# Performance work log

Measured on AMD Instinct MI355X. Metric: run time of the kernel, lower is better.

The kernel has to match this reference:

```python
import jax, jax.numpy as jnp
import numpy as np

DIM = 256
NUM_HEADS = 8
WH, WW = 7, 7
N = WH * WW
HEAD_DIM = DIM // NUM_HEADS
SCALE = HEAD_DIM ** -0.5
B_ = 4096
NW = 64  # windows per image


def _relative_position_index():
    # Swin relative position index: (N, N) int32 in [0, (2Wh-1)*(2Ww-1))
    coords = np.stack(np.meshgrid(np.arange(WH), np.arange(WW), indexing='ij'))  # (2, Wh, Ww)
    cf = coords.reshape(2, -1)  # (2, N)
    rel = cf[:, :, None] - cf[:, None, :]  # (2, N, N)
    rel = rel.transpose(1, 2, 0).copy()
    rel[:, :, 0] += WH - 1
    rel[:, :, 1] += WW - 1
    rel[:, :, 0] *= 2 * WW - 1
    return jnp.asarray(rel.sum(-1), dtype=jnp.int32)  # (N, N)


def setup_inputs() -> dict:
    key = jax.random.key(0)
    ks = jax.random.split(key, 7)
    x = jax.random.normal(ks[0], (B_, N, DIM), dtype=jnp.float32)
    mask = jax.random.normal(ks[1], (NW, N, N), dtype=jnp.float32)
    qkv_w = jax.random.normal(ks[2], (3 * DIM, DIM), dtype=jnp.float32) * 0.02
    qkv_b = jnp.zeros((3 * DIM,), dtype=jnp.float32)
    proj_w = jax.random.normal(ks[3], (DIM, DIM), dtype=jnp.float32) * 0.02
    proj_b = jnp.zeros((DIM,), dtype=jnp.float32)
    bias_table = jax.random.normal(ks[4], ((2 * WH - 1) * (2 * WW - 1), NUM_HEADS), dtype=jnp.float32) * 0.02
    rel_index = _relative_position_index()
    return {"x": x, "mask": mask, "qkv_w": qkv_w, "qkv_b": qkv_b,
            "proj_w": proj_w, "proj_b": proj_b, "bias_table": bias_table,
            "rel_index": rel_index}


def reference(x, mask, qkv_w, qkv_b, proj_w, proj_b, bias_table, rel_index):
    Bw, n, c = x.shape
    # qkv projection: (B_, N, 3C) -> (3, B_, nH, N, hd)
    qkv = (x @ qkv_w.T + qkv_b).reshape(Bw, n, 3, NUM_HEADS, HEAD_DIM)
    qkv = qkv.transpose(2, 0, 3, 1, 4)
    q, k, v = qkv[0], qkv[1], qkv[2]
    attn = jnp.einsum('bhqd,bhkd->bhqk', q * SCALE, k)  # (B_, nH, N, N)
    # gathered relative position bias: (nH, N, N)
    rpb = bias_table[rel_index.reshape(-1)].reshape(n, n, NUM_HEADS).transpose(2, 0, 1)
    attn = attn + rpb[None]
    # window mask: reshape batch into (B, nW) and broadcast mask per-window
    nW = mask.shape[0]
    attn = attn.reshape(Bw // nW, nW, NUM_HEADS, n, n) + mask[None, :, None]
    attn = attn.reshape(Bw, NUM_HEADS, n, n)
    attn = jax.nn.softmax(attn, axis=-1)
    out = jnp.einsum('bhqk,bhkd->bhqd', attn, v)  # (B_, nH, N, hd)
    out = out.transpose(0, 2, 1, 3).reshape(Bw, n, c)
    return out @ proj_w.T + proj_b
```

## Files before the change

### kernel.cpp

```cpp
#include <hip/hip_runtime.h>
#include <hip/hip_bf16.h>

typedef __bf16 bf16;
typedef __bf16 bf16x2 __attribute__((ext_vector_type(2)));
typedef __bf16 bf16x8 __attribute__((ext_vector_type(8)));
typedef float  f32x4  __attribute__((ext_vector_type(4)));
typedef float  f32x8  __attribute__((ext_vector_type(8)));

#define MFMA16(A,B,C) __builtin_amdgcn_mfma_f32_16x16x32_bf16((A),(B),(C),0,0,0)

constexpr int   N_TOK = 49;
constexpr int   DIM_C = 256;
constexpr float SCALE = 0.17677669529663687f;

constexpr int VT         = 25088;
constexpr int PAD_BASE   = VT + 256 * 56;
constexpr int SMEM_ELEMS = PAD_BASE + 512;

constexpr size_t CB_BYTES    = 64ull * 8 * 64 * 64 * 4;
constexpr int    QKVW_ELEMS  = 768 * 256;
constexpr int    PROJW_ELEMS = 256 * 256;

__global__ __launch_bounds__(256) void build_cb_kernel(
    const float* __restrict__ bias_table, const float* __restrict__ mask,
    const int* __restrict__ rel_index, float* __restrict__ cb) {
  int idx = blockIdx.x * 256 + threadIdx.x;
  int j = idx & 63, m = (idx >> 6) & 63, h = (idx >> 12) & 7, w = idx >> 15;
  float v = 0.f;
  if (j < N_TOK && m < N_TOK)
    v = bias_table[rel_index[m * 49 + j] * 8 + h] + mask[(w * 49 + m) * 49 + j];
  cb[idx] = v;
}

__global__ __launch_bounds__(256) void cvt_w_kernel(
    const float* __restrict__ qkv_w, const float* __restrict__ proj_w,
    bf16* __restrict__ qkv_wb, bf16* __restrict__ proj_wb) {
  int i = blockIdx.x * 256 + threadIdx.x;
  if (i < QKVW_ELEMS) qkv_wb[i] = (bf16)qkv_w[i];
  else                proj_wb[i - QKVW_ELEMS] = (bf16)proj_w[i - QKVW_ELEMS];
}

__global__ __launch_bounds__(512, 4) void win_attn_kernel(
    const float* __restrict__ x, const bf16* __restrict__ qkv_wb,
    const float* __restrict__ qkv_b, const bf16* __restrict__ proj_wb,
    const float* __restrict__ proj_b, const float* __restrict__ cb,
    float* __restrict__ out) {
  __shared__ bf16 smem[SMEM_ELEMS];

  const int beta  = blockIdx.x;
  const int w_idx = beta >> 6;
  const int img   = beta & 63;
  const int b     = img * 64 + w_idx;
  const int tid   = threadIdx.x;
  const int wv    = tid >> 6;
  const int l     = tid & 63;
  const int l15   = l & 15, lgp = l >> 4;

  const f32x4 fzero = {0.f, 0.f, 0.f, 0.f};

  if (tid < 512) smem[PAD_BASE + tid] = (bf16)0.f;
  if (tid < 224) {
    int d = 224 + tid / 7, j = 49 + tid % 7;
    smem[VT + d * 56 + j] = (bf16)0.f;
  }

  const float* xg = x + (size_t)b * (N_TOK * DIM_C);
  for (int c = tid; c < (N_TOK * DIM_C / 8); c += 512) {
    int m = c >> 5, k0 = (c & 31) * 8;
    f32x8 f = *reinterpret_cast<const f32x8*>(xg + m * 256 + k0);
    bf16x8 v;
#pragma unroll
    for (int e = 0; e < 8; ++e) v[e] = (bf16)f[e];
    *reinterpret_cast<bf16x8*>(&smem[VT + m * 256 + (k0 ^ ((m & 7) << 3))]) = v;
  }
  __syncthreads();

  {
    f32x4 acc[4][4];
#pragma unroll
    for (int i = 0; i < 4; ++i)
      for (int mt = 0; mt < 4; ++mt) acc[i][mt] = fzero;
    for (int k0 = 0; k0 < 8; ++k0) {
      const int kk = k0 * 32 + lgp * 8;
      bf16x8 XBf[4];
#pragma unroll
      for (int mt = 0; mt < 4; ++mt) {
        int m = mt * 16 + l15; int mc = m < N_TOK ? m : 48;
        XBf[mt] = *reinterpret_cast<const bf16x8*>(
            &smem[VT + mc * 256 + (kk ^ ((mc & 7) << 3))]);
      }
#pragma unroll
      for (int i = 0; i < 4; ++i) {
        int c = (4 * wv + i) * 16 + l15;
        bf16x8 Aw = *reinterpret_cast<const bf16x8*>(qkv_wb + c * DIM_C + kk);
#pragma unroll
        for (int mt = 0; mt < 4; ++mt) acc[i][mt] = MFMA16(Aw, XBf[mt], acc[i][mt]);
      }
    }
#pragma unroll
    for (int i = 0; i < 4; ++i) {
      int ct = 4 * wv + i;
      int c0 = ct * 16 + lgp * 4;
      f32x4 qb = *reinterpret_cast<const f32x4*>(qkv_b + c0);
      float sc = (ct < 16) ? SCALE : 1.0f;
#pragma unroll
      for (int mt = 0; mt < 4; ++mt) {
        int m = mt * 16 + l15;
        if (m < N_TOK) {
          float v0 = (acc[i][mt][0] + qb[0]) * sc;
          float v1 = (acc[i][mt][1] + qb[1]) * sc;
          float v2 = (acc[i][mt][2] + qb[2]) * sc;
          float v3 = (acc[i][mt][3] + qb[3]) * sc;
          int base = m * 512 + (c0 ^ ((m & 7) << 3));
          *reinterpret_cast<bf16x2*>(&smem[base])     = bf16x2{(bf16)v0, (bf16)v1};
          *reinterpret_cast<bf16x2*>(&smem[base + 2]) = bf16x2{(bf16)v2, (bf16)v3};
        }
      }
    }
  }

  {
    f32x4 accv[2][4];
#pragma unroll
    for (int i = 0; i < 2; ++i)
      for (int mt = 0; mt < 4; ++mt) accv[i][mt] = fzero;
    for (int k0 = 0; k0 < 8; ++k0) {
      const int kk = k0 * 32 + lgp * 8;
      bf16x8 XA[4];
#pragma unroll
      for (int mt = 0; mt < 4; ++mt) {
        int m = mt * 16 + l15; int mc = m < N_TOK ? m : 48;
        XA[mt] = *reinterpret_cast<const bf16x8*>(
            &smem[VT + mc * 256 + (kk ^ ((mc & 7) << 3))]);
      }
#pragma unroll
      for (int i = 0; i < 2; ++i) {
        int c = (32 + 2 * wv + i) * 16 + l15;
        bf16x8 Bw = *reinterpret_cast<const bf16x8*>(qkv_wb + c * DIM_C + kk);
#pragma unroll
        for (int mt = 0; mt < 4; ++mt) accv[i][mt] = MFMA16(XA[mt], Bw, accv[i][mt]);
      }
    }
    __syncthreads();
#pragma unroll
    for (int i = 0; i < 2; ++i) {
      int dd = (2 * wv + i) * 16 + l15;
      float qb = qkv_b[512 + dd];
#pragma unroll
      for (int mt = 0; mt < 4; ++mt) {
#pragma unroll
        for (int r = 0; r < 4; ++r) {
          int m = mt * 16 + lgp * 4 + r;
          if (m < N_TOK) smem[VT + dd * 56 + m] = (bf16)(accv[i][mt][r] + qb);
        }
      }
    }
  }
  __syncthreads();

  const int h = wv;
  {
    bf16x8 Vf[2][2];
#pragma unroll
    for (int dt = 0; dt < 2; ++dt)
#pragma unroll
      for (int ks = 0; ks < 2; ++ks) {
        int d = h * 32 + dt * 16 + l15;
        Vf[dt][ks] = *reinterpret_cast<const bf16x8*>(
            &smem[VT + d * 56 + ks * 32 + lgp * 8]);
      }
    bf16x8 Ak[4];
#pragma unroll
    for (int jt = 0; jt < 4; ++jt) {
      int j = jt * 16 + l15; int jr = j < N_TOK ? j : 48;
      Ak[jt] = *reinterpret_cast<const bf16x8*>(
          &smem[jr * 512 + ((256 + h * 32 + lgp * 8) ^ ((jr & 7) << 3))]);
    }
    const float* cbp = cb + ((size_t)(w_idx * 8 + h)) * 4096;

#pragma unroll
    for (int mt = 0; mt < 4; ++mt) {
      int mrow = mt * 16 + l15;
      int mc = mrow < N_TOK ? mrow : 48;
      bf16x8 Bq = *reinterpret_cast<const bf16x8*>(
          &smem[mc * 512 + ((h * 32 + lgp * 8) ^ ((mc & 7) << 3))]);
      f32x4 s4[4];
#pragma unroll
      for (int jt = 0; jt < 4; ++jt) s4[jt] = MFMA16(Ak[jt], Bq, fzero);

      float e[4][4];
#pragma unroll
      for (int jt = 0; jt < 4; ++jt) {
        f32x4 cb4 = *reinterpret_cast<const f32x4*>(
            cbp + mrow * 64 + jt * 16 + lgp * 4);
#pragma unroll
        for (int r = 0; r < 4; ++r) {
          float v = s4[jt][r] + cb4[r];
          if (jt == 3) {
            if (r == 0) v = (lgp == 0) ? v : -3.0e38f;
            else        v = -3.0e38f;
          }
          e[jt][r] = v;
        }
      }
      float mx = e[0][0];
#pragma unroll
      for (int jt = 0; jt < 4; ++jt)
#pragma unroll
        for (int r = 0; r < 4; ++r) mx = fmaxf(mx, e[jt][r]);
      mx = fmaxf(mx, __shfl_xor(mx, 16));
      mx = fmaxf(mx, __shfl_xor(mx, 32));
      float sum = 0.f;
#pragma unroll
      for (int jt = 0; jt < 4; ++jt)
#pragma unroll
        for (int r = 0; r < 4; ++r) {
          float ex = __expf(e[jt][r] - mx);
          e[jt][r] = ex;
          sum += ex;
        }
      sum += __shfl_xor(sum, 16);
      sum += __shfl_xor(sum, 32);
      float rinv = 1.0f / sum;

      if (mrow < N_TOK) {
#pragma unroll
        for (int jt = 0; jt < 4; ++jt) {
          int jc0 = jt * 16 + lgp * 4;
          int cc  = (jt < 2) ? (h * 32 + jc0) : (224 + h * 32 + jc0);
          int base = mrow * 512 + (cc ^ ((mrow & 7) << 3));
          *reinterpret_cast<bf16x2*>(&smem[base]) =
              bf16x2{(bf16)e[jt][0], (bf16)e[jt][1]};
          *reinterpret_cast<bf16x2*>(&smem[base + 2]) =
              bf16x2{(bf16)e[jt][2], (bf16)e[jt][3]};
        }
      }
      f32x4 pv[2] = {fzero, fzero};
#pragma unroll
      for (int ks = 0; ks < 2; ++ks) {
        int j0 = ks * 32 + lgp * 8;
        int cc = ((ks == 0) ? (h * 32) : (224 + h * 32)) + j0;
        bf16x8 Bp = *reinterpret_cast<const bf16x8*>(
            &smem[mc * 512 + (cc ^ ((mc & 7) << 3))]);
#pragma unroll
        for (int dt = 0; dt < 2; ++dt) pv[dt] = MFMA16(Vf[dt][ks], Bp, pv[dt]);
      }
      if (mrow < N_TOK) {
#pragma unroll
        for (int dt = 0; dt < 2; ++dt) {
          float a0 = pv[dt][0] * rinv, a1 = pv[dt][1] * rinv;
          float a2 = pv[dt][2] * rinv, a3 = pv[dt][3] * rinv;
          int cc0 = 256 + h * 32 + dt * 16 + lgp * 4;
          int base = mrow * 512 + (cc0 ^ ((mrow & 7) << 3));
          *reinterpret_cast<bf16x2*>(&smem[base])     = bf16x2{(bf16)a0, (bf16)a1};
          *reinterpret_cast<bf16x2*>(&smem[base + 2]) = bf16x2{(bf16)a2, (bf16)a3};
        }
      }
    }
  }
  __syncthreads();

  f32x4 acc2[2][4];
#pragma unroll
  for (int ci = 0; ci < 2; ++ci)
    for (int mt = 0; mt < 4; ++mt) acc2[ci][mt] = fzero;
  for (int k0 = 0; k0 < 8; ++k0) {
    const int kk = k0 * 32 + lgp * 8;
    bf16x8 Bao[4];
#pragma unroll
    for (int mt = 0; mt < 4; ++mt) {
      int m = mt * 16 + l15; int mc = m < N_TOK ? m : 48;
      Bao[mt] = *reinterpret_cast<const bf16x8*>(
          &smem[mc * 512 + ((256 + kk) ^ ((mc & 7) << 3))]);
    }
#pragma unroll
    for (int ci = 0; ci < 2; ++ci) {
      int c = (2 * wv + ci) * 16 + l15;
      bf16x8 Aw = *reinterpret_cast<const bf16x8*>(proj_wb + c * DIM_C + kk);
#pragma unroll
      for (int mt = 0; mt < 4; ++mt) acc2[ci][mt] = MFMA16(Aw, Bao[mt], acc2[ci][mt]);
    }
  }
  float* ob = out + (size_t)b * (N_TOK * DIM_C);
#pragma unroll
  for (int ci = 0; ci < 2; ++ci) {
    int c0 = (2 * wv + ci) * 16 + lgp * 4;
    f32x4 pb = *reinterpret_cast<const f32x4*>(proj_b + c0);
#pragma unroll
    for (int mt = 0; mt < 4; ++mt) {
      int mrow = mt * 16 + l15;
      if (mrow < N_TOK) {
        f32x4 o;
#pragma unroll
        for (int r = 0; r < 4; ++r) o[r] = acc2[ci][mt][r] + pb[r];
        *reinterpret_cast<f32x4*>(ob + mrow * 256 + c0) = o;
      }
    }
  }
}

extern "C" void kernel_launch(void* const* d_in, const int* in_sizes, int n_in,
                              void* d_out, int out_size, void* d_ws, size_t ws_size,
                              hipStream_t stream) {
  const float* x          = (const float*)d_in[0];
  const float* mask       = (const float*)d_in[1];
  const float* qkv_w      = (const float*)d_in[2];
  const float* qkv_b      = (const float*)d_in[3];
  const float* proj_w     = (const float*)d_in[4];
  const float* proj_b     = (const float*)d_in[5];
  const float* bias_table = (const float*)d_in[6];
  const int*   rel_index  = (const int*)d_in[7];

  float* cb      = (float*)d_ws;
  bf16*  qkv_wb  = (bf16*)((char*)d_ws + CB_BYTES);
  bf16*  proj_wb = (bf16*)((char*)d_ws + CB_BYTES + QKVW_ELEMS * 2);

  hipLaunchKernelGGL(build_cb_kernel, dim3(8192), dim3(256), 0, stream,
                     bias_table, mask, rel_index, cb);
  hipLaunchKernelGGL(cvt_w_kernel, dim3(1024), dim3(256), 0, stream,
                     qkv_w, proj_w, qkv_wb, proj_wb);
  hipLaunchKernelGGL(win_attn_kernel, dim3(4096), dim3(512), 0, stream,
                     x, qkv_wb, qkv_b, proj_wb, proj_b, cb, (float*)d_out);
}
```

Measured before the change: 427.9 us.

## Keep per-head Q/K/V and P in registers via cross-lane shuffles instead of LDS

```diff
diff --git a/kernel.cpp b/kernel.cpp
--- a/kernel.cpp
+++ b/kernel.cpp
@@ -2,7 +2,7 @@
 #include <hip/hip_bf16.h>
 
 typedef __bf16 bf16;
-typedef __bf16 bf16x2 __attribute__((ext_vector_type(2)));
+typedef __bf16 bf16x4v __attribute__((ext_vector_type(4)));
 typedef __bf16 bf16x8 __attribute__((ext_vector_type(8)));
 typedef float  f32x4  __attribute__((ext_vector_type(4)));
 typedef float  f32x8  __attribute__((ext_vector_type(8)));
@@ -13,9 +13,7 @@
 constexpr int   DIM_C = 256;
 constexpr float SCALE = 0.17677669529663687f;
 
-constexpr int VT         = 25088;
-constexpr int PAD_BASE   = VT + 256 * 56;
-constexpr int SMEM_ELEMS = PAD_BASE + 512;
+constexpr int SMEM_ELEMS = N_TOK * 256;
 
 constexpr size_t CB_BYTES    = 64ull * 8 * 64 * 64 * 4;
 constexpr int    QKVW_ELEMS  = 768 * 256;
@@ -40,6 +38,28 @@
   else                proj_wb[i - QKVW_ELEMS] = (bf16)proj_w[i - QKVW_ELEMS];
 }
 
+__device__ __forceinline__ bf16x8 repack8(f32x4 Ta, f32x4 Tb, int l15, int lgp) {
+  const int s0 = l15 + ((lgp & 1) << 5);
+  const bool hi = (lgp & 2) != 0;
+  bf16x8 F;
+#pragma unroll
+  for (int r = 0; r < 4; ++r) {
+    float a0 = __shfl(Ta[r], s0);
+    float b0 = __shfl(Tb[r], s0);
+    F[r] = (bf16)(hi ? b0 : a0);
+    float a1 = __shfl(Ta[r], s0 + 16);
+    float b1 = __shfl(Tb[r], s0 + 16);
+    F[r + 4] = (bf16)(hi ? b1 : a1);
+  }
+  return F;
+}
+
+__device__ __forceinline__ bf16x8 tile_read(const bf16* sm, int mt, int l15, int kk) {
+  int m = mt * 16 + l15;
+  int mc = m < N_TOK ? m : 48;
+  return *reinterpret_cast<const bf16x8*>(&sm[mc * 256 + (kk ^ ((mc & 7) << 3))]);
+}
+
 __global__ __launch_bounds__(512, 4) void win_attn_kernel(
     const float* __restrict__ x, const bf16* __restrict__ qkv_wb,
     const float* __restrict__ qkv_b, const bf16* __restrict__ proj_wb,
@@ -55,14 +75,9 @@
   const int wv    = tid >> 6;
   const int l     = tid & 63;
   const int l15   = l & 15, lgp = l >> 4;
+  const int h     = wv;
 
   const f32x4 fzero = {0.f, 0.f, 0.f, 0.f};
-
-  if (tid < 512) smem[PAD_BASE + tid] = (bf16)0.f;
-  if (tid < 224) {
-    int d = 224 + tid / 7, j = 49 + tid % 7;
-    smem[VT + d * 56 + j] = (bf16)0.f;
-  }
 
   const float* xg = x + (size_t)b * (N_TOK * DIM_C);
   for (int c = tid; c < (N_TOK * DIM_C / 8); c += 512) {
@@ -71,191 +86,145 @@
     bf16x8 v;
 #pragma unroll
     for (int e = 0; e < 8; ++e) v[e] = (bf16)f[e];
-    *reinterpret_cast<bf16x8*>(&smem[VT + m * 256 + (k0 ^ ((m & 7) << 3))]) = v;
+    *reinterpret_cast<bf16x8*>(&smem[m * 256 + (k0 ^ ((m & 7) << 3))]) = v;
   }
   __syncthreads();
 
+  bf16x8 Qf[4], Kf[4];
   {
-    f32x4 acc[4][4];
-#pragma unroll
-    for (int i = 0; i < 4; ++i)
-      for (int mt = 0; mt < 4; ++mt) acc[i][mt] = fzero;
+    f32x4 dq[2][4], dk[2][4];
+#pragma unroll
+    for (int i = 0; i < 2; ++i)
+      for (int mt = 0; mt < 4; ++mt) { dq[i][mt] = fzero; dk[i][mt] = fzero; }
+#pragma unroll 2
     for (int k0 = 0; k0 < 8; ++k0) {
       const int kk = k0 * 32 + lgp * 8;
-      bf16x8 XBf[4];
-#pragma unroll
-      for (int mt = 0; mt < 4; ++mt) {
-        int m = mt * 16 + l15; int mc = m < N_TOK ? m : 48;
-        XBf[mt] = *reinterpret_cast<const bf16x8*>(
-            &smem[VT + mc * 256 + (kk ^ ((mc & 7) << 3))]);
-      }
-#pragma unroll
-      for (int i = 0; i < 4; ++i) {
-        int c = (4 * wv + i) * 16 + l15;
-        bf16x8 Aw = *reinterpret_cast<const bf16x8*>(qkv_wb + c * DIM_C + kk);
-#pragma unroll
-        for (int mt = 0; mt < 4; ++mt) acc[i][mt] = MFMA16(Aw, XBf[mt], acc[i][mt]);
-      }
-    }
-#pragma unroll
-    for (int i = 0; i < 4; ++i) {
-      int ct = 4 * wv + i;
-      int c0 = ct * 16 + lgp * 4;
-      f32x4 qb = *reinterpret_cast<const f32x4*>(qkv_b + c0);
-      float sc = (ct < 16) ? SCALE : 1.0f;
-#pragma unroll
-      for (int mt = 0; mt < 4; ++mt) {
-        int m = mt * 16 + l15;
-        if (m < N_TOK) {
-          float v0 = (acc[i][mt][0] + qb[0]) * sc;
-          float v1 = (acc[i][mt][1] + qb[1]) * sc;
-          float v2 = (acc[i][mt][2] + qb[2]) * sc;
-          float v3 = (acc[i][mt][3] + qb[3]) * sc;
-          int base = m * 512 + (c0 ^ ((m & 7) << 3));
-          *reinterpret_cast<bf16x2*>(&smem[base])     = bf16x2{(bf16)v0, (bf16)v1};
-          *reinterpret_cast<bf16x2*>(&smem[base + 2]) = bf16x2{(bf16)v2, (bf16)v3};
+      bf16x8 X[4];
+#pragma unroll
+      for (int mt = 0; mt < 4; ++mt) X[mt] = tile_read(smem, mt, l15, kk);
+#pragma unroll
+      for (int i = 0; i < 2; ++i) {
+        int cq = (2 * h + i) * 16 + l15;
+        bf16x8 Aq = *reinterpret_cast<const bf16x8*>(qkv_wb + cq * DIM_C + kk);
+#pragma unroll
+        for (int mt = 0; mt < 4; ++mt) dq[i][mt] = MFMA16(Aq, X[mt], dq[i][mt]);
+        int ck = (16 + 2 * h + i) * 16 + l15;
+        bf16x8 Ak = *reinterpret_cast<const bf16x8*>(qkv_wb + ck * DIM_C + kk);
+#pragma unroll
+        for (int mt = 0; mt < 4; ++mt) dk[i][mt] = MFMA16(Ak, X[mt], dk[i][mt]);
+      }
+    }
+#pragma unroll
+    for (int i = 0; i < 2; ++i) {
+      f32x4 qb = *reinterpret_cast<const f32x4*>(qkv_b + (2 * h + i) * 16 + lgp * 4);
+      f32x4 kb = *reinterpret_cast<const f32x4*>(qkv_b + 256 + (2 * h + i) * 16 + lgp * 4);
+#pragma unroll
+      for (int mt = 0; mt < 4; ++mt)
+#pragma unroll
+        for (int r = 0; r < 4; ++r) {
+          dq[i][mt][r] = (dq[i][mt][r] + qb[r]) * SCALE;
+          dk[i][mt][r] += kb[r];
         }
-      }
-    }
-  }
-
+    }
+#pragma unroll
+    for (int mt = 0; mt < 4; ++mt) Qf[mt] = repack8(dq[0][mt], dq[1][mt], l15, lgp);
+#pragma unroll
+    for (int jt = 0; jt < 4; ++jt) Kf[jt] = repack8(dk[0][jt], dk[1][jt], l15, lgp);
+  }
+
+  bf16x8 Vf[2][2];
   {
-    f32x4 accv[2][4];
+    f32x4 dv[2][4];
 #pragma unroll
     for (int i = 0; i < 2; ++i)
-      for (int mt = 0; mt < 4; ++mt) accv[i][mt] = fzero;
+      for (int mt = 0; mt < 4; ++mt) dv[i][mt] = fzero;
+#pragma unroll 2
     for (int k0 = 0; k0 < 8; ++k0) {
       const int kk = k0 * 32 + lgp * 8;
-      bf16x8 XA[4];
-#pragma unroll
-      for (int mt = 0; mt < 4; ++mt) {
-        int m = mt * 16 + l15; int mc = m < N_TOK ? m : 48;
-        XA[mt] = *reinterpret_cast<const bf16x8*>(
-            &smem[VT + mc * 256 + (kk ^ ((mc & 7) << 3))]);
-      }
+      bf16x8 X[4];
+#pragma unroll
+      for (int mt = 0; mt < 4; ++mt) X[mt] = tile_read(smem, mt, l15, kk);
 #pragma unroll
       for (int i = 0; i < 2; ++i) {
-        int c = (32 + 2 * wv + i) * 16 + l15;
-        bf16x8 Bw = *reinterpret_cast<const bf16x8*>(qkv_wb + c * DIM_C + kk);
-#pragma unroll
-        for (int mt = 0; mt < 4; ++mt) accv[i][mt] = MFMA16(XA[mt], Bw, accv[i][mt]);
+        int cv = (32 + 2 * h + i) * 16 + l15;
+        bf16x8 Bw = *reinterpret_cast<const bf16x8*>(qkv_wb + cv * DIM_C + kk);
+#pragma unroll
+        for (int mt = 0; mt < 4; ++mt) dv[i][mt] = MFMA16(X[mt], Bw, dv[i][mt]);
       }
     }
     __syncthreads();
 #pragma unroll
     for (int i = 0; i < 2; ++i) {
-      int dd = (2 * wv + i) * 16 + l15;
-      float qb = qkv_b[512 + dd];
-#pragma unroll
-      for (int mt = 0; mt < 4; ++mt) {
-#pragma unroll
-        for (int r = 0; r < 4; ++r) {
-          int m = mt * 16 + lgp * 4 + r;
-          if (m < N_TOK) smem[VT + dd * 56 + m] = (bf16)(accv[i][mt][r] + qb);
+      float vb = qkv_b[512 + (32 + 2 * h + i) * 16 + l15 - 512];
+#pragma unroll
+      for (int mt = 0; mt < 4; ++mt)
+#pragma unroll
+        for (int r = 0; r < 4; ++r) dv[i][mt][r] += vb;
+#pragma unroll
+      for (int ks = 0; ks < 2; ++ks)
+        Vf[i][ks] = repack8(dv[i][ks * 2], dv[i][ks * 2 + 1], l15, lgp);
+    }
+  }
+
+  const float* cbp = cb + ((size_t)(w_idx * 8 + h)) * 4096;
+#pragma unroll
+  for (int mt = 0; mt < 4; ++mt) {
+    int mrow = mt * 16 + l15;
+    f32x4 cb4[4];
+#pragma unroll
+    for (int jt = 0; jt < 4; ++jt)
+      cb4[jt] = *reinterpret_cast<const f32x4*>(cbp + mrow * 64 + jt * 16 + lgp * 4);
+    f32x4 e4[4];
+#pragma unroll
+    for (int jt = 0; jt < 4; ++jt) e4[jt] = MFMA16(Kf[jt], Qf[mt], fzero);
+#pragma unroll
+    for (int jt = 0; jt < 4; ++jt)
+#pragma unroll
+      for (int r = 0; r < 4; ++r) {
+        float v = e4[jt][r] + cb4[jt][r];
+        if (jt == 3) {
+          if (r != 0 || lgp != 0) v = -3.0e38f;
         }
-      }
-    }
-  }
-  __syncthreads();
-
-  const int h = wv;
-  {
-    bf16x8 Vf[2][2];
-#pragma unroll
-    for (int dt = 0; dt < 2; ++dt)
-#pragma unroll
-      for (int ks = 0; ks < 2; ++ks) {
-        int d = h * 32 + dt * 16 + l15;
-        Vf[dt][ks] = *reinterpret_cast<const bf16x8*>(
-            &smem[VT + d * 56 + ks * 32 + lgp * 8]);
-      }
-    bf16x8 Ak[4];
-#pragma unroll
-    for (int jt = 0; jt < 4; ++jt) {
-      int j = jt * 16 + l15; int jr = j < N_TOK ? j : 48;
-      Ak[jt] = *reinterpret_cast<const bf16x8*>(
-          &smem[jr * 512 + ((256 + h * 32 + lgp * 8) ^ ((jr & 7) << 3))]);
-    }
-    const float* cbp = cb + ((size_t)(w_idx * 8 + h)) * 4096;
-
-#pragma unroll
-    for (int mt = 0; mt < 4; ++mt) {
-      int mrow = mt * 16 + l15;
-      int mc = mrow < N_TOK ? mrow : 48;
-      bf16x8 Bq = *reinterpret_cast<const bf16x8*>(
-          &smem[mc * 512 + ((h * 32 + lgp * 8) ^ ((mc & 7) << 3))]);
-      f32x4 s4[4];
-#pragma unroll
-      for (int jt = 0; jt < 4; ++jt) s4[jt] = MFMA16(Ak[jt], Bq, fzero);
-
-      float e[4][4];
-#pragma unroll
-      for (int jt = 0; jt < 4; ++jt) {
-        f32x4 cb4 = *reinterpret_cast<const f32x4*>(
-            cbp + mrow * 64 + jt * 16 + lgp * 4);
-#pragma unroll
-        for (int r = 0; r < 4; ++r) {
-          float v = s4[jt][r] + cb4[r];
-          if (jt == 3) {
-            if (r == 0) v = (lgp == 0) ? v : -3.0e38f;
-            else        v = -3.0e38f;
-          }
-          e[jt][r] = v;
-        }
-      }
-      float mx = e[0][0];
-#pragma unroll
-      for (int jt = 0; jt < 4; ++jt)
-#pragma unroll
-        for (int r = 0; r < 4; ++r) mx = fmaxf(mx, e[jt][r]);
-      mx = fmaxf(mx, __shfl_xor(mx, 16));
-      mx = fmaxf(mx, __shfl_xor(mx, 32));
-      float sum = 0.f;
-#pragma unroll
-      for (int jt = 0; jt < 4; ++jt)
-#pragma unroll
-        for (int r = 0; r < 4; ++r) {
-          float ex = __expf(e[jt][r] - mx);
-          e[jt][r] = ex;
-          sum += ex;
-        }
-      sum += __shfl_xor(sum, 16);
-      sum += __shfl_xor(sum, 32);
-      float rinv = 1.0f / sum;
-
-      if (mrow < N_TOK) {
-#pragma unroll
-        for (int jt = 0; jt < 4; ++jt) {
-          int jc0 = jt * 16 + lgp * 4;
-          int cc  = (jt < 2) ? (h * 32 + jc0) : (224 + h * 32 + jc0);
-          int base = mrow * 512 + (cc ^ ((mrow & 7) << 3));
-          *reinterpret_cast<bf16x2*>(&smem[base]) =
-              bf16x2{(bf16)e[jt][0], (bf16)e[jt][1]};
-          *reinterpret_cast<bf16x2*>(&smem[base + 2]) =
-              bf16x2{(bf16)e[jt][2], (bf16)e[jt][3]};
-        }
-      }
-      f32x4 pv[2] = {fzero, fzero};
-#pragma unroll
-      for (int ks = 0; ks < 2; ++ks) {
-        int j0 = ks * 32 + lgp * 8;
-        int cc = ((ks == 0) ? (h * 32) : (224 + h * 32)) + j0;
-        bf16x8 Bp = *reinterpret_cast<const bf16x8*>(
-            &smem[mc * 512 + (cc ^ ((mc & 7) << 3))]);
-#pragma unroll
-        for (int dt = 0; dt < 2; ++dt) pv[dt] = MFMA16(Vf[dt][ks], Bp, pv[dt]);
-      }
-      if (mrow < N_TOK) {
-#pragma unroll
-        for (int dt = 0; dt < 2; ++dt) {
-          float a0 = pv[dt][0] * rinv, a1 = pv[dt][1] * rinv;
-          float a2 = pv[dt][2] * rinv, a3 = pv[dt][3] * rinv;
-          int cc0 = 256 + h * 32 + dt * 16 + lgp * 4;
-          int base = mrow * 512 + (cc0 ^ ((mrow & 7) << 3));
-          *reinterpret_cast<bf16x2*>(&smem[base])     = bf16x2{(bf16)a0, (bf16)a1};
-          *reinterpret_cast<bf16x2*>(&smem[base + 2]) = bf16x2{(bf16)a2, (bf16)a3};
-        }
-      }
+        e4[jt][r] = v;
+      }
+    float mx = e4[0][0];
+#pragma unroll
+    for (int jt = 0; jt < 4; ++jt)
+#pragma unroll
+      for (int r = 0; r < 4; ++r) mx = fmaxf(mx, e4[jt][r]);
+    mx = fmaxf(mx, __shfl_xor(mx, 16));
+    mx = fmaxf(mx, __shfl_xor(mx, 32));
+    float sum = 0.f;
+#pragma unroll
+    for (int jt = 0; jt < 4; ++jt)
+#pragma unroll
+      for (int r = 0; r < 4; ++r) {
+        float ex = __expf(e4[jt][r] - mx);
+        e4[jt][r] = ex;
+        sum += ex;
+      }
+    sum += __shfl_xor(sum, 16);
+    sum += __shfl_xor(sum, 32);
+    float rinv = 1.0f / sum;
+
+    bf16x8 Pf0 = repack8(e4[0], e4[1], l15, lgp);
+    bf16x8 Pf1 = repack8(e4[2], e4[3], l15, lgp);
+    f32x4 pv0 = MFMA16(Vf[0][0], Pf0, fzero);
+    pv0 = MFMA16(Vf[0][1], Pf1, pv0);
+    f32x4 pv1 = MFMA16(Vf[1][0], Pf0, fzero);
+    pv1 = MFMA16(Vf[1][1], Pf1, pv1);
+
+    if (mrow < N_TOK) {
+      bf16x4v w0, w1;
+#pragma unroll
+      for (int r = 0; r < 4; ++r) {
+        w0[r] = (bf16)(pv0[r] * rinv);
+        w1[r] = (bf16)(pv1[r] * rinv);
+      }
+      int sw = (mrow & 7) << 3;
+      int c0 = 32 * h + lgp * 4;
+      *reinterpret_cast<bf16x4v*>(&smem[mrow * 256 + (c0 ^ sw)]) = w0;
+      *reinterpret_cast<bf16x4v*>(&smem[mrow * 256 + ((c0 + 16) ^ sw)]) = w1;
     }
   }
   __syncthreads();
@@ -264,15 +233,12 @@
 #pragma unroll
   for (int ci = 0; ci < 2; ++ci)
     for (int mt = 0; mt < 4; ++mt) acc2[ci][mt] = fzero;
+#pragma unroll 2
   for (int k0 = 0; k0 < 8; ++k0) {
     const int kk = k0 * 32 + lgp * 8;
     bf16x8 Bao[4];
 #pragma unroll
-    for (int mt = 0; mt < 4; ++mt) {
-      int m = mt * 16 + l15; int mc = m < N_TOK ? m : 48;
-      Bao[mt] = *reinterpret_cast<const bf16x8*>(
-          &smem[mc * 512 + ((256 + kk) ^ ((mc & 7) << 3))]);
-    }
+    for (int mt = 0; mt < 4; ++mt) Bao[mt] = tile_read(smem, mt, l15, kk);
 #pragma unroll
     for (int ci = 0; ci < 2; ++ci) {
       int c = (2 * wv + ci) * 16 + l15;
```

New measurement: 511.2 us. +19.5%, slower.
